# Kernel optimization log

Measured on AMD Instinct MI355X. Metric: run time of the kernel, lower is better.

## Reference

```python
import jax, jax.numpy as jnp
import numpy as np

G = 16          # groups
K = 5           # kernel_size
IPG = 1024 // G # in_channels_per_group
OPG = 1024 // G # out_channels_per_group


def setup_inputs() -> dict:
    key = jax.random.key(0)
    k1, k2, k3 = jax.random.split(key, 3)
    inputs = jax.random.normal(k1, (4, 4096, 1024), dtype=jnp.float32)
    positions = jnp.sort(
        jax.random.randint(k2, (4, 4096), 0, 8192, dtype=jnp.int32), axis=-1)
    # kaiming-uniform-like init for kernel [G, OPG, IPG, K]
    fan_in = IPG * K
    bound = float(np.sqrt(6.0 / fan_in))
    kernel = jax.random.uniform(k3, (G, OPG, IPG, K), dtype=jnp.float32,
                                minval=-bound, maxval=bound)
    return {"inputs": inputs, "positions": positions, "kernel": kernel}


def reference(inputs, positions, kernel):
    B, L, C = inputs.shape
    c = K // 2
    # pad sequence dim; pad positions with -1 sentinel (never matches expected)
    pi = jnp.pad(inputs, ((0, 0), (c, c), (0, 0)))            # [B, L+2c, C]
    pp = jnp.pad(positions, ((0, 0), (c, c)), constant_values=-1)  # [B, L+2c]
    # sliding-window gather indices (equivalent to unfold with stride 1)
    idx = jnp.arange(L)[:, None] + jnp.arange(K)[None, :]      # [L, K]
    ip = pi[:, idx, :]        # [B, L, K, C] input patches
    ppatch = pp[:, idx]       # [B, L, K]  position patches
    # center of each patch is the original position at that output index
    offsets = jnp.arange(-c, c + 1, dtype=positions.dtype)    # [K]
    expected = positions[:, :, None] + offsets                # [B, L, K]
    mask = (ppatch == expected).astype(inputs.dtype)          # [B, L, K]
    masked = ip * mask[..., None]                             # [B, L, K, C]
    # split channels into groups: [B, L, K, G, IPG]
    gp = masked.reshape(B, L, K, G, IPG)
    # grouped conv reduce over in_channels_per_group and kernel taps
    out = jnp.einsum('blkgi,goik->blgo', gp, kernel)           # [B, L, G, OPG]
    return out
```

## Files before the change

### kernel.cpp

```cpp
#include <hip/hip_runtime.h>

typedef __attribute__((ext_vector_type(8))) short short8;
typedef __attribute__((ext_vector_type(4))) float float4v;
typedef __attribute__((ext_vector_type(4))) unsigned short us4;
typedef __attribute__((ext_vector_type(4))) unsigned int uint4v;

namespace {
constexpr int NG   = 16;
constexpr int LSEQ = 4096;
constexpr int CIN  = 1024;
constexpr int IPG  = 64;
constexpr int OPG  = 64;
constexpr int KT   = 5;
constexpr int ROWS = 64;
constexpr int SIN_ROWS = ROWS + KT - 1;
constexpr int SIN_SLOTS = SIN_ROWS * 16;
constexpr int KSTEPS = 10;
constexpr size_t WFRAG_SHORTS = (size_t)NG * 4 * KSTEPS * 512;
constexpr size_t WFRAG_BYTES  = WFRAG_SHORTS * 2;
constexpr size_t MASK_BYTES   = (size_t)4 * LSEQ;
}

__device__ __forceinline__ unsigned short f2bf(float f) {
  unsigned int u = __builtin_bit_cast(unsigned int, f);
  u += 0x7fffu + ((u >> 16) & 1u);
  return (unsigned short)(u >> 16);
}

__global__ __launch_bounds__(256) void prep_fused(const float* __restrict__ gwt,
                                                  const int* __restrict__ gpos,
                                                  unsigned short* __restrict__ wfrag,
                                                  unsigned char* __restrict__ gmask) {
  if (blockIdx.x < 160) {
    const int u = blockIdx.x * 256 + threadIdx.x;
    const int E    = u * 8;
    const int tile = E >> 9;
    const int w9   = E & 511;
    const int n    = w9 >> 5;
    const int quad = (w9 & 31) >> 3;
    const int ks   = tile % KSTEPS;
    const int tt   = tile / KSTEPS;
    const int t    = tt & 3;
    const int g    = tt >> 2;
    const int tap  = ks >> 1;
    const int h    = ks & 1;
    const int o    = t * 16 + n;
    const float* src = gwt + (((size_t)(g * 64 + o) * 64) + h * 32 + quad * 8) * KT + tap;
    short8 v;
    #pragma unroll
    for (int j = 0; j < 8; ++j)
      v[j] = (short)f2bf(src[j * KT]);
    *(short8*)(wfrag + E) = v;
  } else {
    const int id = (blockIdx.x - 160) * 256 + threadIdx.x;
    const int b  = id >> 12;
    const int l  = id & (LSEQ - 1);
    const int base = b * LSEQ;
    const int pc = gpos[base + l];
    unsigned int mbits = 0;
    #pragma unroll
    for (int tap = 0; tap < KT; ++tap) {
      const int lsrc = l + tap - 2;
      int ok = 0;
      if (lsrc >= 0 && lsrc < LSEQ)
        ok = (gpos[base + lsrc] == pc + (tap - 2));
      mbits |= (unsigned int)ok << tap;
    }
    gmask[id] = (unsigned char)mbits;
  }
}

__global__ __launch_bounds__(256) void mconv_main7(
    const float* __restrict__ gin,
    const unsigned char* __restrict__ gmask,
    const unsigned short* __restrict__ wfrag,
    float* __restrict__ gout) {
  __shared__ __align__(16) float sIn[SIN_SLOTS * 4];

  const int tid  = threadIdx.x;
  const int wv   = tid >> 6;
  const int lane = tid & 63;
  const int quad = lane >> 4;
  const int l16  = lane & 15;
  const int wm   = wv & 1;
  const int wn   = wv >> 1;

  const int g  = blockIdx.y;
  const int b  = blockIdx.z;
  const int l0 = blockIdx.x * ROWS;
  const int bL = b * LSEQ;

  const float* ginb = gin + (size_t)bL * CIN + g * IPG;

  auto stage_one = [&](int u) {
    const int r  = u >> 4;
    const int ps = u & 15;
    const int c4 = ps ^ (r & 15);
    int l = l0 - 2 + r;
    l = l < 0 ? 0 : (l > LSEQ - 1 ? LSEQ - 1 : l);
    const float* src = ginb + (size_t)l * CIN + c4 * 4;
    __builtin_amdgcn_global_load_lds(
        (const __attribute__((address_space(1))) void*)(const void*)src,
        (__attribute__((address_space(3))) void*)(void*)&sIn[u * 4],
        16, 0, 0);
  };

  #pragma unroll
  for (int k = 0; k < 4; ++k)
    stage_one(tid + k * 256);
  if (wv == 0)
    stage_one(tid + 1024);

  int mb[2];
  #pragma unroll
  for (int mt = 0; mt < 2; ++mt)
    mb[mt] = gmask[bL + l0 + wm * 32 + mt * 16 + l16];

  const int laneoff = l16 * 32 + quad * 8;
  const unsigned short* wb0 = wfrag + (size_t)((g * 4 + wn * 2) * KSTEPS) * 512 + laneoff;
  const unsigned short* wb1 = wb0 + (size_t)KSTEPS * 512;
  const short8 zero8 = {0, 0, 0, 0, 0, 0, 0, 0};
  const float4v zf = {0.f, 0.f, 0.f, 0.f};

  __syncthreads();

  float4v acc[2][2];
  #pragma unroll
  for (int mt = 0; mt < 2; ++mt) { acc[mt][0] = zf; acc[mt][1] = zf; }
  short8 bc0 = *(const short8*)(wb0);
  short8 bc1 = *(const short8*)(wb1);

  #pragma unroll 2
  for (int ks = 0; ks < KSTEPS; ++ks) {
    const int ksn = (ks + 1 < KSTEPS) ? ks + 1 : KSTEPS - 1;
    short8 bn0 = *(const short8*)(wb0 + ksn * 512);
    short8 bn1 = *(const short8*)(wb1 + ksn * 512);
    const int tap = ks >> 1;
    const int h   = ks & 1;
    const int ls  = h * 8 + quad * 2;
    #pragma unroll
    for (int mt = 0; mt < 2; ++mt) {
      const int r   = wm * 32 + mt * 16 + l16 + tap;
      const int swz = r & 15;
      const float* rowp = &sIn[r * 64];
      float4v lo = *(const float4v*)(rowp + ((ls ^ swz) << 2));
      float4v hi = *(const float4v*)(rowp + (((ls + 1) ^ swz) << 2));
      unsigned int d0, d1, d2, d3;
      asm("v_cvt_pk_bf16_f32 %0, %1, %2" : "=v"(d0) : "v"(lo[0]), "v"(lo[1]));
      asm("v_cvt_pk_bf16_f32 %0, %1, %2" : "=v"(d1) : "v"(lo[2]), "v"(lo[3]));
      asm("v_cvt_pk_bf16_f32 %0, %1, %2" : "=v"(d2) : "v"(hi[0]), "v"(hi[1]));
      asm("v_cvt_pk_bf16_f32 %0, %1, %2" : "=v"(d3) : "v"(hi[2]), "v"(hi[3]));
      uint4v dv = {d0, d1, d2, d3};
      short8 a = __builtin_bit_cast(short8, dv);
      if (!((mb[mt] >> tap) & 1)) a = zero8;
      acc[mt][0] = __builtin_amdgcn_mfma_f32_16x16x32_bf16(a, bc0, acc[mt][0], 0, 0, 0);
      acc[mt][1] = __builtin_amdgcn_mfma_f32_16x16x32_bf16(a, bc1, acc[mt][1], 0, 0, 0);
    }
    bc0 = bn0; bc1 = bn1;
  }

  #pragma unroll
  for (int mt = 0; mt < 2; ++mt) {
    const int lrow = l0 + wm * 32 + mt * 16 + quad * 4;
    #pragma unroll
    for (int reg = 0; reg < 4; ++reg) {
      float* orow = gout + (size_t)(bL + lrow + reg) * CIN + g * OPG + wn * 32;
      orow[l16]      = acc[mt][0][reg];
      orow[16 + l16] = acc[mt][1][reg];
    }
  }
}

namespace fb {
constexpr int ROWS_PER_CHUNK = 128;
constexpr int CHUNKS = 4;
constexpr int ROWS_PER_BLOCK = 512;
constexpr int SW_STRIDE  = 328;
constexpr int FSIN_STRIDE = 72;
constexpr int FSIN_ROWS   = 132;
}

__global__ __launch_bounds__(256, 2) void mconv_f32_mfma(
    const float* __restrict__ gin, const int* __restrict__ gpos,
    const float* __restrict__ gwt, float* __restrict__ gout) {
  using namespace fb;
  __shared__ __align__(16) unsigned short sW[OPG * SW_STRIDE];
  __shared__ __align__(16) unsigned short sIn[FSIN_ROWS * FSIN_STRIDE];
  __shared__ unsigned char sMask[ROWS_PER_CHUNK * KT];

  const int tid  = threadIdx.x;
  const int wave = tid >> 6;
  const int lane = tid & 63;
  const int quad = lane >> 4;
  const int l16  = lane & 15;
  const int g  = blockIdx.y;
  const int b  = blockIdx.z;
  const int tile0 = blockIdx.x * ROWS_PER_BLOCK;
  const int bL = b * LSEQ;

  {
    const float* wg = gwt + (size_t)g * (OPG * IPG * KT);
    for (int u = tid; u < (OPG * IPG * KT) / 4; u += 256) {
      const int base = u * 4;
      float4v v = *(const float4v*)(wg + base);
      int o = base / (IPG * KT);
      int r = base - o * (IPG * KT);
      int i = r / KT;
      int k = r - i * KT;
      int addr = o * SW_STRIDE + k * IPG + i;
      #pragma unroll
      for (int t = 0; t < 4; ++t) {
        sW[addr] = f2bf(v[t]);
        ++k; addr += IPG;
        if (k == KT) { k = 0; ++i; addr -= KT * IPG - 1; }
      }
    }
  }
  const short8 zero8 = {0,0,0,0,0,0,0,0};
  const float4v zf = {0.f,0.f,0.f,0.f};
  for (int ch = 0; ch < CHUNKS; ++ch) {
    const int l0 = tile0 + ch * ROWS_PER_CHUNK;
    __syncthreads();
    for (int t = tid; t < ROWS_PER_CHUNK * KT; t += 256) {
      const int lr = t / KT, tap = t - lr * KT, l = l0 + lr, lsrc = l + tap - 2;
      int ok = 0;
      if (lsrc >= 0 && lsrc < LSEQ) ok = (gpos[bL + lsrc] == gpos[bL + l] + (tap - 2));
      sMask[t] = (unsigned char)ok;
    }
    for (int u = tid; u < FSIN_ROWS * 16; u += 256) {
      const int r = u >> 4, c4 = u & 15, l = l0 - 2 + r;
      us4 w = {0,0,0,0};
      if (l >= 0 && l < LSEQ) {
        float4v v = *(const float4v*)(gin + (size_t)(bL + l) * CIN + g * IPG + c4 * 4);
        w[0]=f2bf(v[0]); w[1]=f2bf(v[1]); w[2]=f2bf(v[2]); w[3]=f2bf(v[3]);
      }
      *(us4*)(&sIn[r * FSIN_STRIDE + c4 * 4]) = w;
    }
    __syncthreads();
    float4v acc[2][4];
    #pragma unroll
    for (int mm = 0; mm < 2; ++mm)
      #pragma unroll
      for (int nt = 0; nt < 4; ++nt) acc[mm][nt] = zf;
    const int m0 = wave * 32 + l16, m1 = m0 + 16;
    #pragma unroll
    for (int tap = 0; tap < KT; ++tap) {
      const bool msk0 = sMask[m0 * KT + tap] != 0;
      const bool msk1 = sMask[m1 * KT + tap] != 0;
      #pragma unroll
      for (int h = 0; h < 2; ++h) {
        const int kk = tap * IPG + h * 32 + quad * 8;
        const short8 b0 = *(const short8*)(&sW[(0*16 + l16) * SW_STRIDE + kk]);
        const short8 b1 = *(const short8*)(&sW[(1*16 + l16) * SW_STRIDE + kk]);
        const short8 b2 = *(const short8*)(&sW[(2*16 + l16) * SW_STRIDE + kk]);
        const short8 b3 = *(const short8*)(&sW[(3*16 + l16) * SW_STRIDE + kk]);
        const int ci = h * 32 + quad * 8;
        short8 a0 = *(const short8*)(&sIn[(m0 + tap) * FSIN_STRIDE + ci]);
        short8 a1 = *(const short8*)(&sIn[(m1 + tap) * FSIN_STRIDE + ci]);
        if (!msk0) a0 = zero8;
        if (!msk1) a1 = zero8;
        acc[0][0] = __builtin_amdgcn_mfma_f32_16x16x32_bf16(a0,b0,acc[0][0],0,0,0);
        acc[0][1] = __builtin_amdgcn_mfma_f32_16x16x32_bf16(a0,b1,acc[0][1],0,0,0);
        acc[0][2] = __builtin_amdgcn_mfma_f32_16x16x32_bf16(a0,b2,acc[0][2],0,0,0);
        acc[0][3] = __builtin_amdgcn_mfma_f32_16x16x32_bf16(a0,b3,acc[0][3],0,0,0);
        acc[1][0] = __builtin_amdgcn_mfma_f32_16x16x32_bf16(a1,b0,acc[1][0],0,0,0);
        acc[1][1] = __builtin_amdgcn_mfma_f32_16x16x32_bf16(a1,b1,acc[1][1],0,0,0);
        acc[1][2] = __builtin_amdgcn_mfma_f32_16x16x32_bf16(a1,b2,acc[1][2],0,0,0);
        acc[1][3] = __builtin_amdgcn_mfma_f32_16x16x32_bf16(a1,b3,acc[1][3],0,0,0);
      }
    }
    #pragma unroll
    for (int mm = 0; mm < 2; ++mm) {
      const int lrow = l0 + wave * 32 + mm * 16 + quad * 4;
      #pragma unroll
      for (int reg = 0; reg < 4; ++reg) {
        float* orow = gout + ((size_t)(bL + lrow + reg) * NG + g) * OPG;
        #pragma unroll
        for (int nt = 0; nt < 4; ++nt)
          orow[nt * 16 + l16] = acc[mm][nt][reg];
      }
    }
  }
}

extern "C" void kernel_launch(void* const* d_in, const int* in_sizes, int n_in,
                              void* d_out, int out_size, void* d_ws, size_t ws_size,
                              hipStream_t stream) {
  (void)in_sizes; (void)n_in; (void)out_size;
  const float* gin  = (const float*)d_in[0];
  const int*   gpos = (const int*)d_in[1];
  const float* gwt  = (const float*)d_in[2];
  float*       gout = (float*)d_out;

  if (ws_size >= WFRAG_BYTES + MASK_BYTES) {
    unsigned short* wfrag = (unsigned short*)d_ws;
    unsigned char*  gmask = (unsigned char*)d_ws + WFRAG_BYTES;
    hipLaunchKernelGGL(prep_fused, dim3(224), dim3(256), 0, stream,
                       gwt, gpos, wfrag, gmask);
    dim3 grid(LSEQ / ROWS, NG, 4);
    hipLaunchKernelGGL(mconv_main7, grid, dim3(256), 0, stream,
                       gin, gmask, wfrag, gout);
  } else {
    dim3 grid(LSEQ / fb::ROWS_PER_BLOCK, NG, 4);
    hipLaunchKernelGGL(mconv_f32_mfma, grid, dim3(256), 0, stream,
                       gin, gpos, gwt, gout);
  }
}
```

Before: 136.2 us.

## Give each wave its own 32-row tile with full 64-col output and private LDS

```diff
diff --git a/kernel.cpp b/kernel.cpp
--- a/kernel.cpp
+++ b/kernel.cpp
@@ -12,9 +12,9 @@
 constexpr int IPG  = 64;
 constexpr int OPG  = 64;
 constexpr int KT   = 5;
-constexpr int ROWS = 64;
-constexpr int SIN_ROWS = ROWS + KT - 1;
-constexpr int SIN_SLOTS = SIN_ROWS * 16;
+constexpr int WROWS = 32;
+constexpr int SROWS = WROWS + KT - 1;
+constexpr int WSLOTS = SROWS * 16;
 constexpr int KSTEPS = 10;
 constexpr size_t WFRAG_SHORTS = (size_t)NG * 4 * KSTEPS * 512;
 constexpr size_t WFRAG_BYTES  = WFRAG_SHORTS * 2;
@@ -70,79 +70,82 @@
   }
 }
 
-__global__ __launch_bounds__(256) void mconv_main7(
+__global__ __launch_bounds__(256, 4) void mconv_main8(
     const float* __restrict__ gin,
     const unsigned char* __restrict__ gmask,
     const unsigned short* __restrict__ wfrag,
     float* __restrict__ gout) {
-  __shared__ __align__(16) float sIn[SIN_SLOTS * 4];
+  __shared__ __align__(16) float sIn[4][WSLOTS * 4];
 
   const int tid  = threadIdx.x;
   const int wv   = tid >> 6;
   const int lane = tid & 63;
   const int quad = lane >> 4;
   const int l16  = lane & 15;
-  const int wm   = wv & 1;
-  const int wn   = wv >> 1;
-
-  const int g  = blockIdx.y;
-  const int b  = blockIdx.z;
-  const int l0 = blockIdx.x * ROWS;
-  const int bL = b * LSEQ;
+
+  const int g   = blockIdx.y;
+  const int b   = blockIdx.z;
+  const int l0w = blockIdx.x * (4 * WROWS) + wv * WROWS;
+  const int bL  = b * LSEQ;
 
   const float* ginb = gin + (size_t)bL * CIN + g * IPG;
 
-  auto stage_one = [&](int u) {
+  #pragma unroll
+  for (int k = 0; k < 9; ++k) {
+    const int u  = lane + k * 64;
     const int r  = u >> 4;
     const int ps = u & 15;
     const int c4 = ps ^ (r & 15);
-    int l = l0 - 2 + r;
+    int l = l0w - 2 + r;
     l = l < 0 ? 0 : (l > LSEQ - 1 ? LSEQ - 1 : l);
     const float* src = ginb + (size_t)l * CIN + c4 * 4;
     __builtin_amdgcn_global_load_lds(
         (const __attribute__((address_space(1))) void*)(const void*)src,
-        (__attribute__((address_space(3))) void*)(void*)&sIn[u * 4],
+        (__attribute__((address_space(3))) void*)(void*)&sIn[wv][u * 4],
         16, 0, 0);
-  };
-
-  #pragma unroll
-  for (int k = 0; k < 4; ++k)
-    stage_one(tid + k * 256);
-  if (wv == 0)
-    stage_one(tid + 1024);
+  }
 
   int mb[2];
   #pragma unroll
   for (int mt = 0; mt < 2; ++mt)
-    mb[mt] = gmask[bL + l0 + wm * 32 + mt * 16 + l16];
+    mb[mt] = gmask[bL + l0w + mt * 16 + l16];
 
   const int laneoff = l16 * 32 + quad * 8;
-  const unsigned short* wb0 = wfrag + (size_t)((g * 4 + wn * 2) * KSTEPS) * 512 + laneoff;
-  const unsigned short* wb1 = wb0 + (size_t)KSTEPS * 512;
+  const unsigned short* wb[4];
+  #pragma unroll
+  for (int nt = 0; nt < 4; ++nt)
+    wb[nt] = wfrag + (size_t)((g * 4 + nt) * KSTEPS) * 512 + laneoff;
+
+  short8 bc[4], bn[4];
+  #pragma unroll
+  for (int nt = 0; nt < 4; ++nt)
+    bc[nt] = *(const short8*)(wb[nt]);
+
   const short8 zero8 = {0, 0, 0, 0, 0, 0, 0, 0};
   const float4v zf = {0.f, 0.f, 0.f, 0.f};
-
-  __syncthreads();
-
-  float4v acc[2][2];
-  #pragma unroll
-  for (int mt = 0; mt < 2; ++mt) { acc[mt][0] = zf; acc[mt][1] = zf; }
-  short8 bc0 = *(const short8*)(wb0);
-  short8 bc1 = *(const short8*)(wb1);
+  float4v acc[2][4];
+  #pragma unroll
+  for (int mt = 0; mt < 2; ++mt)
+    #pragma unroll
+    for (int nt = 0; nt < 4; ++nt) acc[mt][nt] = zf;
+
+  asm volatile("s_waitcnt vmcnt(0)" ::: "memory");
+  __builtin_amdgcn_sched_barrier(0);
 
   #pragma unroll 2
   for (int ks = 0; ks < KSTEPS; ++ks) {
     const int ksn = (ks + 1 < KSTEPS) ? ks + 1 : KSTEPS - 1;
-    short8 bn0 = *(const short8*)(wb0 + ksn * 512);
-    short8 bn1 = *(const short8*)(wb1 + ksn * 512);
+    #pragma unroll
+    for (int nt = 0; nt < 4; ++nt)
+      bn[nt] = *(const short8*)(wb[nt] + ksn * 512);
     const int tap = ks >> 1;
     const int h   = ks & 1;
     const int ls  = h * 8 + quad * 2;
     #pragma unroll
     for (int mt = 0; mt < 2; ++mt) {
-      const int r   = wm * 32 + mt * 16 + l16 + tap;
-      const int swz = r & 15;
-      const float* rowp = &sIn[r * 64];
+      const int lr  = mt * 16 + l16 + tap;
+      const int swz = lr & 15;
+      const float* rowp = &sIn[wv][lr * 64];
       float4v lo = *(const float4v*)(rowp + ((ls ^ swz) << 2));
       float4v hi = *(const float4v*)(rowp + (((ls + 1) ^ swz) << 2));
       unsigned int d0, d1, d2, d3;
@@ -153,20 +156,24 @@
       uint4v dv = {d0, d1, d2, d3};
       short8 a = __builtin_bit_cast(short8, dv);
       if (!((mb[mt] >> tap) & 1)) a = zero8;
-      acc[mt][0] = __builtin_amdgcn_mfma_f32_16x16x32_bf16(a, bc0, acc[mt][0], 0, 0, 0);
-      acc[mt][1] = __builtin_amdgcn_mfma_f32_16x16x32_bf16(a, bc1, acc[mt][1], 0, 0, 0);
-    }
-    bc0 = bn0; bc1 = bn1;
+      acc[mt][0] = __builtin_amdgcn_mfma_f32_16x16x32_bf16(a, bc[0], acc[mt][0], 0, 0, 0);
+      acc[mt][1] = __builtin_amdgcn_mfma_f32_16x16x32_bf16(a, bc[1], acc[mt][1], 0, 0, 0);
+      acc[mt][2] = __builtin_amdgcn_mfma_f32_16x16x32_bf16(a, bc[2], acc[mt][2], 0, 0, 0);
+      acc[mt][3] = __builtin_amdgcn_mfma_f32_16x16x32_bf16(a, bc[3], acc[mt][3], 0, 0, 0);
+    }
+    #pragma unroll
+    for (int nt = 0; nt < 4; ++nt) bc[nt] = bn[nt];
   }
 
   #pragma unroll
   for (int mt = 0; mt < 2; ++mt) {
-    const int lrow = l0 + wm * 32 + mt * 16 + quad * 4;
+    const int lrow = l0w + mt * 16 + quad * 4;
     #pragma unroll
     for (int reg = 0; reg < 4; ++reg) {
-      float* orow = gout + (size_t)(bL + lrow + reg) * CIN + g * OPG + wn * 32;
-      orow[l16]      = acc[mt][0][reg];
-      orow[16 + l16] = acc[mt][1][reg];
+      float* orow = gout + (size_t)(bL + lrow + reg) * CIN + g * OPG;
+      #pragma unroll
+      for (int nt = 0; nt < 4; ++nt)
+        orow[nt * 16 + l16] = acc[mt][nt][reg];
     }
   }
 }
@@ -297,8 +304,8 @@
     unsigned char*  gmask = (unsigned char*)d_ws + WFRAG_BYTES;
     hipLaunchKernelGGL(prep_fused, dim3(224), dim3(256), 0, stream,
                        gwt, gpos, wfrag, gmask);
-    dim3 grid(LSEQ / ROWS, NG, 4);
-    hipLaunchKernelGGL(mconv_main7, grid, dim3(256), 0, stream,
+    dim3 grid(LSEQ / (4 * WROWS), NG, 4);
+    hipLaunchKernelGGL(mconv_main8, grid, dim3(256), 0, stream,
                        gin, gmask, wfrag, gout);
   } else {
     dim3 grid(LSEQ / fb::ROWS_PER_BLOCK, NG, 4);
```

Result: no change. 136.5 us (+0.2%).

## Load activations directly from global memory instead of staging through LDS

Applied to the files above, without the earlier changes.

```diff
diff --git a/kernel.cpp b/kernel.cpp
--- a/kernel.cpp
+++ b/kernel.cpp
@@ -12,9 +12,6 @@
 constexpr int IPG  = 64;
 constexpr int OPG  = 64;
 constexpr int KT   = 5;
-constexpr int ROWS = 64;
-constexpr int SIN_ROWS = ROWS + KT - 1;
-constexpr int SIN_SLOTS = SIN_ROWS * 16;
 constexpr int KSTEPS = 10;
 constexpr size_t WFRAG_SHORTS = (size_t)NG * 4 * KSTEPS * 512;
 constexpr size_t WFRAG_BYTES  = WFRAG_SHORTS * 2;
@@ -70,13 +67,11 @@
   }
 }
 
-__global__ __launch_bounds__(256) void mconv_main7(
+__global__ __launch_bounds__(256) void mconv_main9(
     const float* __restrict__ gin,
     const unsigned char* __restrict__ gmask,
     const unsigned short* __restrict__ wfrag,
     float* __restrict__ gout) {
-  __shared__ __align__(16) float sIn[SIN_SLOTS * 4];
-
   const int tid  = threadIdx.x;
   const int wv   = tid >> 6;
   const int lane = tid & 63;
@@ -87,29 +82,10 @@
 
   const int g  = blockIdx.y;
   const int b  = blockIdx.z;
-  const int l0 = blockIdx.x * ROWS;
+  const int l0 = blockIdx.x * 64;
   const int bL = b * LSEQ;
 
-  const float* ginb = gin + (size_t)bL * CIN + g * IPG;
-
-  auto stage_one = [&](int u) {
-    const int r  = u >> 4;
-    const int ps = u & 15;
-    const int c4 = ps ^ (r & 15);
-    int l = l0 - 2 + r;
-    l = l < 0 ? 0 : (l > LSEQ - 1 ? LSEQ - 1 : l);
-    const float* src = ginb + (size_t)l * CIN + c4 * 4;
-    __builtin_amdgcn_global_load_lds(
-        (const __attribute__((address_space(1))) void*)(const void*)src,
-        (__attribute__((address_space(3))) void*)(void*)&sIn[u * 4],
-        16, 0, 0);
-  };
-
-  #pragma unroll
-  for (int k = 0; k < 4; ++k)
-    stage_one(tid + k * 256);
-  if (wv == 0)
-    stage_one(tid + 1024);
+  const float* ginb = gin + (size_t)bL * CIN + g * IPG + quad * 8;
 
   int mb[2];
   #pragma unroll
@@ -119,32 +95,35 @@
   const int laneoff = l16 * 32 + quad * 8;
   const unsigned short* wb0 = wfrag + (size_t)((g * 4 + wn * 2) * KSTEPS) * 512 + laneoff;
   const unsigned short* wb1 = wb0 + (size_t)KSTEPS * 512;
+
   const short8 zero8 = {0, 0, 0, 0, 0, 0, 0, 0};
   const float4v zf = {0.f, 0.f, 0.f, 0.f};
-
-  __syncthreads();
-
   float4v acc[2][2];
   #pragma unroll
   for (int mt = 0; mt < 2; ++mt) { acc[mt][0] = zf; acc[mt][1] = zf; }
+
   short8 bc0 = *(const short8*)(wb0);
   short8 bc1 = *(const short8*)(wb1);
 
-  #pragma unroll 2
+  int lbase[2];
+  #pragma unroll
+  for (int mt = 0; mt < 2; ++mt)
+    lbase[mt] = l0 + wm * 32 + mt * 16 + l16 - 2;
+
+  #pragma unroll
   for (int ks = 0; ks < KSTEPS; ++ks) {
     const int ksn = (ks + 1 < KSTEPS) ? ks + 1 : KSTEPS - 1;
     short8 bn0 = *(const short8*)(wb0 + ksn * 512);
     short8 bn1 = *(const short8*)(wb1 + ksn * 512);
     const int tap = ks >> 1;
     const int h   = ks & 1;
-    const int ls  = h * 8 + quad * 2;
     #pragma unroll
     for (int mt = 0; mt < 2; ++mt) {
-      const int r   = wm * 32 + mt * 16 + l16 + tap;
-      const int swz = r & 15;
-      const float* rowp = &sIn[r * 64];
-      float4v lo = *(const float4v*)(rowp + ((ls ^ swz) << 2));
-      float4v hi = *(const float4v*)(rowp + (((ls + 1) ^ swz) << 2));
+      int l = lbase[mt] + tap;
+      l = l < 0 ? 0 : (l > LSEQ - 1 ? LSEQ - 1 : l);
+      const float* p = ginb + (size_t)l * CIN + h * 32;
+      float4v lo = *(const float4v*)(p);
+      float4v hi = *(const float4v*)(p + 4);
       unsigned int d0, d1, d2, d3;
       asm("v_cvt_pk_bf16_f32 %0, %1, %2" : "=v"(d0) : "v"(lo[0]), "v"(lo[1]));
       asm("v_cvt_pk_bf16_f32 %0, %1, %2" : "=v"(d1) : "v"(lo[2]), "v"(lo[3]));
@@ -297,8 +276,8 @@
     unsigned char*  gmask = (unsigned char*)d_ws + WFRAG_BYTES;
     hipLaunchKernelGGL(prep_fused, dim3(224), dim3(256), 0, stream,
                        gwt, gpos, wfrag, gmask);
-    dim3 grid(LSEQ / ROWS, NG, 4);
-    hipLaunchKernelGGL(mconv_main7, grid, dim3(256), 0, stream,
+    dim3 grid(LSEQ / 64, NG, 4);
+    hipLaunchKernelGGL(mconv_main9, grid, dim3(256), 0, stream,
                        gin, gmask, wfrag, gout);
   } else {
     dim3 grid(LSEQ / fb::ROWS_PER_BLOCK, NG, 4);
```

New measurement: 194.9 us. +43.1%, slower.
